# Performance work log

Measured on AMD Instinct MI355X. Metric: run time of the kernel, lower is better.

Reference implementation:

```python
import jax, jax.numpy as jnp
from jax import lax
import numpy as np
from functools import partial

B, N, T, H, L = 16, 256, 4, 128, 2
VOCAB, OUT_VOCAB, MAX_STEPS = 1000, 1000, 15


def setup_inputs() -> dict:
    key = jax.random.key(0)
    ks = jax.random.split(key, 13)
    data = jax.random.randint(ks[0], (B, N, T), 0, VOCAB)
    true_branch_nodes = jax.random.randint(ks[1], (B, N), 0, N)
    false_branch_nodes = jax.random.randint(ks[2], (B, N), 0, N)
    exit_index = jax.random.randint(ks[3], (B,), 0, N)
    steps = jax.random.randint(ks[4], (B,), 1, MAX_STEPS + 1)
    s_in = 1.0 / np.sqrt(H)
    s_cat = 1.0 / np.sqrt(2 * L * H)
    embed = jax.random.uniform(ks[5], (VOCAB, H), jnp.float32, -0.1, 0.1)
    Wi = jax.random.normal(ks[6], (L, H, 4 * H), jnp.float32) * s_in
    Wh = jax.random.normal(ks[7], (L, H, 4 * H), jnp.float32) * s_in
    b_lstm = jnp.zeros((L, 4 * H), jnp.float32)
    Wb = jax.random.normal(ks[8], (2 * L * H, 2), jnp.float32) * s_cat
    bb = jax.random.normal(ks[9], (2,), jnp.float32) * 1e-6
    Wo = jax.random.normal(ks[10], (2 * L * H, OUT_VOCAB), jnp.float32) * s_cat
    bo = jax.random.normal(ks[11], (OUT_VOCAB,), jnp.float32) * 1e-6
    return dict(data=data, true_branch_nodes=true_branch_nodes,
                false_branch_nodes=false_branch_nodes, exit_index=exit_index,
                steps=steps, embed=embed, Wi=Wi, Wh=Wh, b_lstm=b_lstm,
                Wb=Wb, bb=bb, Wo=Wo, bo=bo)


def _lstm_step(Wi_l, Wh_l, b_l, c, h, x):
    # flax LSTMCell math: gates from input (no bias) + recurrent (bias)
    z = x @ Wi_l + h @ Wh_l + b_l  # [..., 4H]
    i, f, g, o = jnp.split(z, 4, axis=-1)
    c2 = jax.nn.sigmoid(f) * c + jax.nn.sigmoid(i) * jnp.tanh(g)
    h2 = jax.nn.sigmoid(o) * jnp.tanh(c2)
    return c2, h2


def _forward(data, true_branch_nodes, false_branch_nodes, exit_index, steps,
             embed, Wi, Wh, b_lstm, Wb, bb, Wo, bo):
    emb = embed[data]                       # [B, N, T, H]
    cs = jnp.zeros((L, B, N, H), embed.dtype)
    hs = jnp.zeros((L, B, N, H), embed.dtype)
    ip = jnp.zeros((B, N), embed.dtype).at[:, 0].set(1.0)
    b_idx = jnp.arange(B)

    seg_b = jax.vmap(partial(jax.ops.segment_sum, num_segments=N))        # [B,N,...] , [B,N]
    seg_lb = jax.vmap(seg_b, in_axes=(0, None))                           # [L,B,N,H]

    def execute(cs, hs):
        # run the stacked LSTM over the T statement tokens at every node
        def tok_step(carry, x_t):
            cs, hs = carry
            inp = x_t
            nc, nh = [], []
            for l in range(L):
                c2, h2 = _lstm_step(Wi[l], Wh[l], b_lstm[l], cs[l], hs[l], inp)
                nc.append(c2); nh.append(h2)
                inp = h2
            return (jnp.stack(nc), jnp.stack(nh)), None
        (cs, hs), _ = lax.scan(tok_step, (cs, hs), jnp.moveaxis(emb, 2, 0))
        return cs, hs

    def step(carry, _):
        cs, hs, ip, idx = carry
        cs_c, hs_c = execute(cs, hs)
        # exit node keeps its previous hidden state
        cs_c = cs_c.at[:, b_idx, exit_index].set(cs[:, b_idx, exit_index])
        hs_c = hs_c.at[:, b_idx, exit_index].set(hs[:, b_idx, exit_index])
        # branch decision from concatenated (c, h) of every layer: [B, N, 2LH]
        feats = jnp.concatenate([x for l in range(L) for x in (cs_c[l], hs_c[l])], axis=-1)
        branch = jax.nn.softmax(feats @ Wb + bb, axis=-1)
        wt = branch[..., 0] * ip            # [B, N]
        wf = branch[..., 1] * ip
        ip_new = seg_b(wt, true_branch_nodes) + seg_b(wf, false_branch_nodes)
        denom = (ip_new + 1e-7)[None, :, :, None]
        def agg(h):
            return (seg_lb(h * wt[None, :, :, None], true_branch_nodes)
                    + seg_lb(h * wf[None, :, :, None], false_branch_nodes)) / denom
        cs_new, hs_new = agg(cs_c), agg(hs_c)
        live = idx < steps                   # [B]
        cs = jnp.where(live[None, :, None, None], cs_new, cs)
        hs = jnp.where(live[None, :, None, None], hs_new, hs)
        ip = jnp.where(live[:, None], ip_new, ip)
        return (cs, hs, ip, idx + 1), None

    (cs, hs, ip, _), _ = lax.scan(step, (cs, hs, ip, jnp.zeros((), jnp.int32)),
                                  None, length=MAX_STEPS)
    fc = cs[:, b_idx, exit_index]           # [L, B, H]
    fh = hs[:, b_idx, exit_index]
    final = jnp.concatenate([x for l in range(L) for x in (fc[l], fh[l])], axis=-1)
    logits = final @ Wo + bo                # [B, OUT_VOCAB]
    return logits[:, None, :]


def reference(data, true_branch_nodes, false_branch_nodes, exit_index, steps,
              embed, Wi, Wh, b_lstm, Wb, bb, Wo, bo):
    return _forward(data, true_branch_nodes, false_branch_nodes, exit_index,
                    steps, embed, Wi, Wh, b_lstm, Wb, bb, Wo, bo)
```

## Files before the change

kernel.cpp:

```cpp
#include <hip/hip_runtime.h>
#include <hip/hip_bf16.h>
#include <stdint.h>
#include <stddef.h>

static constexpr int BB = 16, NN = 256, TT = 4, HH = 128;
static constexpr int MM = BB * NN;
static constexpr int CC = 512;
static constexpr int OUTV = 1000;
static constexpr int MAXS = 15;
static constexpr int SP = 132;

typedef float f32x4 __attribute__((ext_vector_type(4)));
typedef short s16x8 __attribute__((ext_vector_type(8)));

__device__ __forceinline__ float sigf(float x) { return 1.0f / (1.0f + __expf(-x)); }
__device__ __forceinline__ float tanhr(float x) { return 2.0f / (1.0f + __expf(-2.0f * x)) - 1.0f; }
__device__ __forceinline__ unsigned short f2bu(float a) {
  return __builtin_bit_cast(unsigned short, __float2bfloat16(a));
}
__device__ __forceinline__ unsigned int packh(float a, float b) {
  return (unsigned int)f2bu(a) | ((unsigned int)f2bu(b) << 16);
}
__device__ __forceinline__ float blo(unsigned int u) { return __builtin_bit_cast(float, u << 16); }
__device__ __forceinline__ float bhi(unsigned int u) { return __builtin_bit_cast(float, u & 0xffff0000u); }


__global__ __launch_bounds__(512) void csr_kernel(const int* __restrict__ tb,
                                                  const int* __restrict__ fb,
                                                  int* __restrict__ offs,
                                                  int* __restrict__ edges) {
  const int blk = blockIdx.x;
  const int tid = threadIdx.x;
  __shared__ int cnt[256], sc[256], cur[256];
  if (tid < 256) cnt[tid] = 0;
  __syncthreads();
  const int n = tid >> 1, bit = tid & 1;
  const int tgt = bit ? fb[blk * NN + n] : tb[blk * NN + n];
  atomicAdd(&cnt[tgt], 1);
  __syncthreads();
  if (tid < 256) sc[tid] = cnt[tid];
  __syncthreads();
  for (int ofs = 1; ofs < 256; ofs <<= 1) {
    int t2 = (tid < 256 && tid >= ofs) ? sc[tid - ofs] : 0;
    __syncthreads();
    if (tid < 256) sc[tid] += t2;
    __syncthreads();
  }
  if (tid < 256) { offs[blk * NN + tid] = blk * 2 * NN + sc[tid] - cnt[tid]; cur[tid] = 0; }
  if (blk == 0 && tid == 0) offs[MM] = 2 * MM;
  __syncthreads();
  int lpos = sc[tgt] - cnt[tgt] + atomicAdd(&cur[tgt], 1);
  edges[blk * 2 * NN + lpos] = (n << 1) | bit;
}

__global__ __launch_bounds__(256) void prep_kernel(
    const float* __restrict__ Wh0, const float* __restrict__ Wi1, const float* __restrict__ Wh1,
    const float* __restrict__ embed, const float* __restrict__ Wi0, const float* __restrict__ b0,
    unsigned short* __restrict__ swz, float* __restrict__ tab) {
  const int blk = blockIdx.x;
  const int tid = threadIdx.x;
  if (blk < 768) {
    int i = blk * 256 + tid;
    int mtx = i >> 16, ii = i & 65535;
    const float* W = (mtx == 0) ? Wh0 : (mtx == 1) ? Wi1 : Wh1;
    int j = ii & 7, ln = (ii >> 3) & 63, kb = (ii >> 9) & 3, ct = ii >> 11;
    int n = ln & 15, q = ln >> 4;
    swz[i] = f2bu(W[(kb * 32 + q * 8 + j) * CC + ct * 16 + n]);
    return;
  }
  const int v0 = (blk - 768) * 8;
  __shared__ float A[8][HH];
  for (int s = tid; s < 8 * HH; s += 256) {
    int r = s >> 7, k = s & 127;
    A[r][k] = embed[(size_t)(v0 + r) * HH + k];
  }
  __syncthreads();
  const int j = tid;
  float za[8], zb[8];
  {
    float ba = b0[j], bbv = b0[j + 256];
#pragma unroll
    for (int r = 0; r < 8; ++r) { za[r] = ba; zb[r] = bbv; }
  }
#pragma unroll 4
  for (int k = 0; k < HH; ++k) {
    float wa = Wi0[k * CC + j], wb = Wi0[k * CC + j + 256];
#pragma unroll
    for (int r = 0; r < 8; ++r) { za[r] += A[r][k] * wa; zb[r] += A[r][k] * wb; }
  }
  const int T = j >> 4, nn2 = j & 15;
  const int base1 = (T & 7) * 64 + nn2 * 4 + (T >> 3);
#pragma unroll
  for (int r = 0; r < 8; ++r) {
    tab[(size_t)(v0 + r) * CC + base1] = za[r];
    tab[(size_t)(v0 + r) * CC + base1 + 2] = zb[r];
  }
}


__global__ __launch_bounds__(512) void step_kernel(
    float* __restrict__ Sc0g, float* __restrict__ Sh0g,
    float* __restrict__ Sc1g, float* __restrict__ Sh1g,
    const unsigned int* __restrict__ Pr, unsigned int* __restrict__ Pw,
    const float* __restrict__ w2R, float* __restrict__ w2W,
    const int* __restrict__ offs, const int* __restrict__ edges,
    const float* __restrict__ tab,
    const unsigned short* __restrict__ swzWh0, const unsigned short* __restrict__ swzWi1,
    const unsigned short* __restrict__ swzWh1, const float* __restrict__ b1,
    const float* __restrict__ Wb, const float* __restrict__ bb,
    const int* __restrict__ data, const int* __restrict__ exi,
    const int* __restrict__ steps, int step) {
  const int B = blockIdx.x;
  const int b = (B & 7) | (((B >> 3) & 1) << 3);
  const int g16 = B >> 4;
  const int row0 = b * NN + g16 * 16;
  const int sb = steps[b];
  const bool aggLive = (step >= 1) && ((step - 1) < sb);
  const bool lstmLive = (step < sb);
  if (!aggLive && !lstmLive) return;

  const int tid = threadIdx.x;
  const int w = tid >> 6;
  const int lane = tid & 63;
  const int n16 = lane & 15, qq = lane >> 4;
  const int kcol = w * 16 + n16;
  const int basePos = ((kcol >> 5) * 64 + ((kcol >> 3) & 3) * 16) * 8 + (kcol & 7);

  __shared__ float c0L[16 * SP], h0L[16 * SP], c1L[16 * SP], h1L[16 * SP];
  __shared__ __align__(16) unsigned short hA0[2][2048], hA1[2][2048];
  __shared__ float exitP[512];
  __shared__ float ipL[16];
  __shared__ int toks[64];

  s16x8 B0f[4][4], B1f[4][4];
  float b1v[4];
  const s16x8* pWh0 = (const s16x8*)swzWh0;
  const s16x8* pWh1 = (const s16x8*)swzWh1;
  const s16x8* pWi1 = (const s16x8*)swzWi1;
  if (lstmLive) {
#pragma unroll
    for (int g = 0; g < 4; ++g) {
      int ci = w + 8 * g;
#pragma unroll
      for (int kb = 0; kb < 4; ++kb) {
        B0f[g][kb] = pWh0[(ci * 4 + kb) * 64 + lane];
        B1f[g][kb] = pWh1[(ci * 4 + kb) * 64 + lane];
      }
      b1v[g] = b1[ci * 16 + n16];
    }
    if (tid < 64) toks[tid] = data[(row0 + (tid >> 2)) * TT + (tid & 3)];
  }

  if (aggLive) {
    const int l = tid & 31;
    const int m = tid >> 5;
    const int node = row0 + m;
    const int beg = offs[node], end = offs[node + 1];
    const float* wR = w2R + (b << 9);
    float ac0[4] = {0,0,0,0}, ah0[4] = {0,0,0,0}, ac1[4] = {0,0,0,0}, ah1[4] = {0,0,0,0};
    float wsum = 0.f;
    float wvA = 0.f, wvB = 0.f;
    uint4 pA0 = {0,0,0,0}, pA1 = {0,0,0,0}, pB0 = {0,0,0,0}, pB1 = {0,0,0,0};
    if (beg < end) {
      int rec = edges[beg];
      wvA = wR[rec];
      const uint4* pr = (const uint4*)(Pr + (size_t)((b << 8) + (rec >> 1)) * 256 + 8 * l);
      pA0 = pr[0]; pA1 = pr[1];
    }
    if (beg + 1 < end) {
      int rec = edges[beg + 1];
      wvB = wR[rec];
      const uint4* pr = (const uint4*)(Pr + (size_t)((b << 8) + (rec >> 1)) * 256 + 8 * l);
      pB0 = pr[0]; pB1 = pr[1];
    }
    for (int e = beg; e < end; e += 2) {
      float w0 = wvA; uint4 u00 = pA0, u01 = pA1;
      float w1 = wvB; uint4 u10 = pB0, u11 = pB1;
      const bool has1 = (e + 1 < end);
      if (e + 2 < end) {
        int rec = edges[e + 2];
        wvA = wR[rec];
        const uint4* pr = (const uint4*)(Pr + (size_t)((b << 8) + (rec >> 1)) * 256 + 8 * l);
        pA0 = pr[0]; pA1 = pr[1];
      }
      if (e + 3 < end) {
        int rec = edges[e + 3];
        wvB = wR[rec];
        const uint4* pr = (const uint4*)(Pr + (size_t)((b << 8) + (rec >> 1)) * 256 + 8 * l);
        pB0 = pr[0]; pB1 = pr[1];
      }
      wsum += w0;
      ac0[0] += w0 * blo(u00.x); ac0[1] += w0 * bhi(u00.x);
      ac0[2] += w0 * blo(u00.y); ac0[3] += w0 * bhi(u00.y);
      ah0[0] += w0 * blo(u00.z); ah0[1] += w0 * bhi(u00.z);
      ah0[2] += w0 * blo(u00.w); ah0[3] += w0 * bhi(u00.w);
      ac1[0] += w0 * blo(u01.x); ac1[1] += w0 * bhi(u01.x);
      ac1[2] += w0 * blo(u01.y); ac1[3] += w0 * bhi(u01.y);
      ah1[0] += w0 * blo(u01.z); ah1[1] += w0 * bhi(u01.z);
      ah1[2] += w0 * blo(u01.w); ah1[3] += w0 * bhi(u01.w);
      if (has1) {
        wsum += w1;
        ac0[0] += w1 * blo(u10.x); ac0[1] += w1 * bhi(u10.x);
        ac0[2] += w1 * blo(u10.y); ac0[3] += w1 * bhi(u10.y);
        ah0[0] += w1 * blo(u10.z); ah0[1] += w1 * bhi(u10.z);
        ah0[2] += w1 * blo(u10.w); ah0[3] += w1 * bhi(u10.w);
        ac1[0] += w1 * blo(u11.x); ac1[1] += w1 * bhi(u11.x);
        ac1[2] += w1 * blo(u11.y); ac1[3] += w1 * bhi(u11.y);
        ah1[0] += w1 * blo(u11.z); ah1[1] += w1 * bhi(u11.z);
        ah1[2] += w1 * blo(u11.w); ah1[3] += w1 * bhi(u11.w);
      }
    }
    float inv = 1.0f / (wsum + 1e-7f);
    float4 o0 = { ac0[0]*inv, ac0[1]*inv, ac0[2]*inv, ac0[3]*inv };
    float4 o1 = { ah0[0]*inv, ah0[1]*inv, ah0[2]*inv, ah0[3]*inv };
    float4 o2 = { ac1[0]*inv, ac1[1]*inv, ac1[2]*inv, ac1[3]*inv };
    float4 o3 = { ah1[0]*inv, ah1[1]*inv, ah1[2]*inv, ah1[3]*inv };
    ((float4*)c0L)[m * (SP / 4) + l] = o0;
    ((float4*)h0L)[m * (SP / 4) + l] = o1;
    ((float4*)c1L)[m * (SP / 4) + l] = o2;
    ((float4*)h1L)[m * (SP / 4) + l] = o3;
    if (l == 0) ipL[m] = wsum;
    if (!lstmLive) {
      ((float4*)Sc0g)[node * 32 + l] = o0;
      ((float4*)Sh0g)[node * 32 + l] = o1;
      ((float4*)Sc1g)[node * 32 + l] = o2;
      ((float4*)Sh1g)[node * 32 + l] = o3;
    }
  } else {
    for (int i2 = tid; i2 < 16 * HH; i2 += 512) {
      int m = i2 >> 7, k = i2 & 127;
      c0L[m * SP + k] = 0.f; h0L[m * SP + k] = 0.f;
      c1L[m * SP + k] = 0.f; h1L[m * SP + k] = 0.f;
    }
    if (tid < 16) ipL[tid] = (((row0 + tid) & (NN - 1)) == 0) ? 1.0f : 0.0f;
  }
  if (!lstmLive) return;

  const int exnode = exi[b];
  const int exm = exnode - (g16 * 16);
  __syncthreads();

  const f32x4* ptab = (const f32x4*)tab;
  f32x4 tvAll[4][4];
#pragma unroll
  for (int t = 0; t < TT; ++t)
#pragma unroll
    for (int r = 0; r < 4; ++r)
      tvAll[t][r] = ptab[(size_t)toks[(qq * 4 + r) * 4 + t] * (CC / 4) + w * 16 + n16];

  if (exm >= 0 && exm < 16 && tid < 128) {
    exitP[tid] = c0L[exm * SP + tid];
    exitP[128 + tid] = h0L[exm * SP + tid];
    exitP[256 + tid] = c1L[exm * SP + tid];
    exitP[384 + tid] = h1L[exm * SP + tid];
  }

  float c0r[4], c1r[4], h0r[4], h1r[4];
#pragma unroll
  for (int r = 0; r < 4; ++r) {
    int m = qq * 4 + r;
    c0r[r] = c0L[m * SP + kcol];
    c1r[r] = c1L[m * SP + kcol];
    h0r[r] = h0L[m * SP + kcol];
    h1r[r] = h1L[m * SP + kcol];
    hA0[0][basePos + m * 8] = f2bu(h0r[r]);
    hA1[0][basePos + m * 8] = f2bu(h1r[r]);
  }
  __syncthreads();

  int cur = 0;
#pragma unroll
  for (int t = 0; t < TT; ++t) {
    const int nxt = cur ^ 1;
    const s16x8* hA0c = (const s16x8*)hA0[cur];
    s16x8 a0[4];
#pragma unroll
    for (int kb = 0; kb < 4; ++kb) a0[kb] = hA0c[kb * 64 + lane];
    f32x4 d0[4];
#pragma unroll
    for (int g = 0; g < 4; ++g)
#pragma unroll
      for (int r = 0; r < 4; ++r)
        d0[g][r] = tvAll[t][r][g];

#pragma unroll
    for (int g = 0; g < 4; ++g)
#pragma unroll
      for (int kb = 0; kb < 4; ++kb)
        d0[g] = __builtin_amdgcn_mfma_f32_16x16x32_bf16(a0[kb], B0f[g][kb], d0[g], 0, 0, 0);

#pragma unroll
    for (int r = 0; r < 4; ++r) {
      float cn = sigf(d0[1][r]) * c0r[r] + sigf(d0[0][r]) * tanhr(d0[2][r]);
      float hn = sigf(d0[3][r]) * tanhr(cn);
      c0r[r] = cn; h0r[r] = hn;
      hA0[nxt][basePos + (qq * 4 + r) * 8] = f2bu(hn);
    }
    __syncthreads();

    const s16x8* hA0n = (const s16x8*)hA0[nxt];
    const s16x8* hA1c = (const s16x8*)hA1[cur];
    s16x8 a1a[4], a1b[4];
#pragma unroll
    for (int kb = 0; kb < 4; ++kb) {
      a1a[kb] = hA0n[kb * 64 + lane];
      a1b[kb] = hA1c[kb * 64 + lane];
    }
    f32x4 d1[4];
#pragma unroll
    for (int g = 0; g < 4; ++g) {
      int ci = w + 8 * g;
      s16x8 wi[4];
#pragma unroll
      for (int kb = 0; kb < 4; ++kb) wi[kb] = pWi1[(ci * 4 + kb) * 64 + lane];
      f32x4 d = { b1v[g], b1v[g], b1v[g], b1v[g] };
#pragma unroll
      for (int kb = 0; kb < 4; ++kb)
        d = __builtin_amdgcn_mfma_f32_16x16x32_bf16(a1a[kb], wi[kb], d, 0, 0, 0);
#pragma unroll
      for (int kb = 0; kb < 4; ++kb)
        d = __builtin_amdgcn_mfma_f32_16x16x32_bf16(a1b[kb], B1f[g][kb], d, 0, 0, 0);
      d1[g] = d;
    }

#pragma unroll
    for (int r = 0; r < 4; ++r) {
      float cn = sigf(d1[1][r]) * c1r[r] + sigf(d1[0][r]) * tanhr(d1[2][r]);
      float hn = sigf(d1[3][r]) * tanhr(cn);
      c1r[r] = cn; h1r[r] = hn;
      if (t + 1 < TT) hA1[nxt][basePos + (qq * 4 + r) * 8] = f2bu(hn);
    }
    cur = nxt;
  }

#pragma unroll
  for (int r = 0; r < 4; ++r) {
    int m = qq * 4 + r;
    c0L[m * SP + kcol] = c0r[r];
    h0L[m * SP + kcol] = h0r[r];
    c1L[m * SP + kcol] = c1r[r];
    h1L[m * SP + kcol] = h1r[r];
  }
  __syncthreads();

  {
    const int m = tid >> 5, sub = tid & 31;
    const int row = row0 + m;
    const bool isExit = (m == exm);
    float z0 = 0.f, z1 = 0.f;
#pragma unroll
    for (int u = 0; u < 16; ++u) {
      int k = u * 32 + sub;
      int seg = k >> 7, kk = k & 127;
      float fk;
      if (isExit) {
        fk = exitP[seg * 128 + kk];
      } else {
        fk = (seg == 0) ? c0L[m * SP + kk] : (seg == 1) ? h0L[m * SP + kk]
           : (seg == 2) ? c1L[m * SP + kk] : h1L[m * SP + kk];
      }
      z0 += fk * Wb[2 * k];
      z1 += fk * Wb[2 * k + 1];
    }
#pragma unroll
    for (int off = 16; off >= 1; off >>= 1) {
      z0 += __shfl_xor(z0, off);
      z1 += __shfl_xor(z1, off);
    }
    if (sub == 0) {
      z0 += bb[0]; z1 += bb[1];
      float mx = fmaxf(z0, z1);
      float e0 = __expf(z0 - mx), e1 = __expf(z1 - mx);
      float inv = 1.0f / (e0 + e1);
      float ipv = ipL[m];
      float2 wp = { e0 * inv * ipv, e1 * inv * ipv };
      ((float2*)w2W)[row] = wp;
    }
  }

  {
    const int m = tid >> 5, l = tid & 31;
    const bool ex = (m == exm);
    const int grow = row0 + m;
    float f0[4], f1[4], f2[4], f3[4];
#pragma unroll
    for (int i = 0; i < 4; ++i) {
      int k = 4 * l + i;
      f0[i] = ex ? exitP[k] : c0L[m * SP + k];
      f1[i] = ex ? exitP[128 + k] : h0L[m * SP + k];
      f2[i] = ex ? exitP[256 + k] : c1L[m * SP + k];
      f3[i] = ex ? exitP[384 + k] : h1L[m * SP + k];
    }
    uint4 o0 = { packh(f0[0], f0[1]), packh(f0[2], f0[3]),
                 packh(f1[0], f1[1]), packh(f1[2], f1[3]) };
    uint4 o1 = { packh(f2[0], f2[1]), packh(f2[2], f2[3]),
                 packh(f3[0], f3[1]), packh(f3[2], f3[3]) };
    uint4* pw = (uint4*)(Pw + (size_t)grow * 256 + 8 * l);
    pw[0] = o0; pw[1] = o1;
  }
}

__global__ void final_kernel(const float* __restrict__ Sc0, const float* __restrict__ Sh0,
                             const float* __restrict__ Sc1, const float* __restrict__ Sh1,
                             const int* __restrict__ exi, const float* __restrict__ Wo,
                             const float* __restrict__ bo, float* __restrict__ out) {
  const int b = blockIdx.x >> 2;
  const int vt = blockIdx.x & 3;
  const int tid = threadIdx.x;
  __shared__ float f[512];
  int row = b * NN + exi[b];
  if (tid < 128) {
    size_t g = (size_t)row * HH + tid;
    f[tid] = Sc0[g];
    f[128 + tid] = Sh0[g];
    f[256 + tid] = Sc1[g];
    f[384 + tid] = Sh1[g];
  }
  __syncthreads();
  if (tid < 250) {
    int v = vt * 250 + tid;
    float acc = bo[v];
#pragma unroll 8
    for (int k = 0; k < 512; ++k) acc += f[k] * Wo[(size_t)k * OUTV + v];
    out[b * OUTV + v] = acc;
  }
}

__global__ void zero_out_kernel(float* __restrict__ out, int n) {
  int i = blockIdx.x * blockDim.x + threadIdx.x;
  if (i < n) out[i] = 0.0f;
}


extern "C" void kernel_launch(void* const* d_in, const int* in_sizes, int n_in,
                              void* d_out, int out_size, void* d_ws, size_t ws_size,
                              hipStream_t stream) {
  const int* data = (const int*)d_in[0];
  const int* tb   = (const int*)d_in[1];
  const int* fb   = (const int*)d_in[2];
  const int* exi  = (const int*)d_in[3];
  const int* steps = (const int*)d_in[4];
  const float* embed = (const float*)d_in[5];
  const float* Wi = (const float*)d_in[6];
  const float* Wh = (const float*)d_in[7];
  const float* bl = (const float*)d_in[8];
  const float* Wb = (const float*)d_in[9];
  const float* bb = (const float*)d_in[10];
  const float* Wo = (const float*)d_in[11];
  const float* bo = (const float*)d_in[12];
  float* out = (float*)d_out;

  const float* Wi0 = Wi;
  const float* Wi1 = Wi + HH * CC;
  const float* Wh0 = Wh;
  const float* Wh1 = Wh + HH * CC;
  const float* b0 = bl;
  const float* b1 = bl + CC;

  float* ws = (float*)d_ws;
  size_t off = 0;
  float* tab = ws + off;  off += (size_t)1024 * CC;
  float* Sc0 = ws + off;  off += (size_t)MM * HH;
  float* Sh0 = ws + off;  off += (size_t)MM * HH;
  float* Sc1 = ws + off;  off += (size_t)MM * HH;
  float* Sh1 = ws + off;  off += (size_t)MM * HH;
  unsigned int* PA = (unsigned int*)(ws + off); off += (size_t)MM * 256;
  unsigned int* PB = (unsigned int*)(ws + off); off += (size_t)MM * 256;
  unsigned short* swz = (unsigned short*)(ws + off); off += 3 * 32768;
  float* w2A = ws + off;  off += 2 * MM;
  float* w2B = ws + off;  off += 2 * MM;
  int* offs  = (int*)(ws + off); off += MM + 16;
  int* edges = (int*)(ws + off); off += 2 * MM;
  (void)in_sizes; (void)n_in; (void)out_size;

  if (ws_size < off * sizeof(float)) {
    zero_out_kernel<<<(BB * OUTV + 255) / 256, 256, 0, stream>>>(out, BB * OUTV);
    return;
  }

  unsigned short* swzWh0 = swz;
  unsigned short* swzWi1 = swz + 65536;
  unsigned short* swzWh1 = swz + 2 * 65536;

  csr_kernel<<<BB, 512, 0, stream>>>(tb, fb, offs, edges);
  prep_kernel<<<893, 256, 0, stream>>>(Wh0, Wi1, Wh1, embed, Wi0, b0, swz, tab);

  for (int s = 0; s <= MAXS; ++s) {
    unsigned int* Pwp = (s & 1) ? PB : PA;
    const unsigned int* Prp = (s & 1) ? PA : PB;
    float* w2Wp = (s & 1) ? w2B : w2A;
    const float* w2Rp = (s & 1) ? w2A : w2B;
    step_kernel<<<MM / 16, 512, 0, stream>>>(
        Sc0, Sh0, Sc1, Sh1, Prp, Pwp,
        w2Rp, w2Wp,
        offs, edges, tab, swzWh0, swzWi1, swzWh1, b1, Wb, bb,
        data, exi, steps, s);
  }
  final_kernel<<<BB * 4, 256, 0, stream>>>(Sc0, Sh0, Sc1, Sh1, exi, Wo, bo, out);
}
```

Measured before the change: 510.0 us.

## Fuse two recurrence steps per launch with per-batch global spin barrier

Each launch now runs two consecutive graph steps instead of one, which halves the number of kernel launches. The two steps are separated by a per-batch counter barrier in global memory: the 16 blocks of each batch increment a slot, and thread 0 of each block spins on it with a timeout. State and weight buffers are read and written through relaxed agent-scope 64-bit atomics, so the data crosses between blocks through the shared cache rather than stale per-CU caches. This costs narrower loads and stores, adds spin-wait latency, and depends on all 16 blocks of a batch being resident at the same time. If the timeout ever fires, results could be wrong.

```diff
diff --git a/kernel.cpp b/kernel.cpp
--- a/kernel.cpp
+++ b/kernel.cpp
@@ -9,9 +9,11 @@
 static constexpr int OUTV = 1000;
 static constexpr int MAXS = 15;
 static constexpr int SP = 132;
+static constexpr int ND = 8;
 
 typedef float f32x4 __attribute__((ext_vector_type(4)));
 typedef short s16x8 __attribute__((ext_vector_type(8)));
+typedef unsigned long long u64;
 
 __device__ __forceinline__ float sigf(float x) { return 1.0f / (1.0f + __expf(-x)); }
 __device__ __forceinline__ float tanhr(float x) { return 2.0f / (1.0f + __expf(-2.0f * x)) - 1.0f; }
@@ -24,14 +26,26 @@
 __device__ __forceinline__ float blo(unsigned int u) { return __builtin_bit_cast(float, u << 16); }
 __device__ __forceinline__ float bhi(unsigned int u) { return __builtin_bit_cast(float, u & 0xffff0000u); }
 
+__device__ __forceinline__ u64 ld64_llc(const u64* p) {
+  return __hip_atomic_load(p, __ATOMIC_RELAXED, __HIP_MEMORY_SCOPE_AGENT);
+}
+__device__ __forceinline__ void st64_llc(u64* p, u64 v) {
+  __hip_atomic_store(p, v, __ATOMIC_RELAXED, __HIP_MEMORY_SCOPE_AGENT);
+}
+__device__ __forceinline__ float ldf_llc(const float* p) {
+  return __hip_atomic_load(p, __ATOMIC_RELAXED, __HIP_MEMORY_SCOPE_AGENT);
+}
+
 
 __global__ __launch_bounds__(512) void csr_kernel(const int* __restrict__ tb,
                                                   const int* __restrict__ fb,
                                                   int* __restrict__ offs,
-                                                  int* __restrict__ edges) {
+                                                  int* __restrict__ edges,
+                                                  unsigned int* __restrict__ bar) {
   const int blk = blockIdx.x;
   const int tid = threadIdx.x;
   __shared__ int cnt[256], sc[256], cur[256];
+  if (tid < ND) bar[tid * 16 + blk] = 0;
   if (tid < 256) cnt[tid] = 0;
   __syncthreads();
   const int n = tid >> 1, bit = tid & 1;
@@ -98,26 +112,29 @@
 }
 
 
-__global__ __launch_bounds__(512) void step_kernel(
+__global__ __launch_bounds__(512) void step2_kernel(
     float* __restrict__ Sc0g, float* __restrict__ Sh0g,
     float* __restrict__ Sc1g, float* __restrict__ Sh1g,
-    const unsigned int* __restrict__ Pr, unsigned int* __restrict__ Pw,
-    const float* __restrict__ w2R, float* __restrict__ w2W,
+    unsigned int* __restrict__ PA, unsigned int* __restrict__ PB,
+    float* __restrict__ w2A, float* __restrict__ w2B,
     const int* __restrict__ offs, const int* __restrict__ edges,
     const float* __restrict__ tab,
     const unsigned short* __restrict__ swzWh0, const unsigned short* __restrict__ swzWi1,
     const unsigned short* __restrict__ swzWh1, const float* __restrict__ b1,
     const float* __restrict__ Wb, const float* __restrict__ bb,
     const int* __restrict__ data, const int* __restrict__ exi,
-    const int* __restrict__ steps, int step) {
+    const int* __restrict__ steps, unsigned int* __restrict__ bar, int d) {
   const int B = blockIdx.x;
   const int b = (B & 7) | (((B >> 3) & 1) << 3);
   const int g16 = B >> 4;
   const int row0 = b * NN + g16 * 16;
   const int sb = steps[b];
-  const bool aggLive = (step >= 1) && ((step - 1) < sb);
-  const bool lstmLive = (step < sb);
-  if (!aggLive && !lstmLive) return;
+  const int s0 = 2 * d;
+  {
+    const bool aggA = (s0 >= 1) && ((s0 - 1) < sb);
+    const bool lstmA = (s0 < sb);
+    if (!aggA && !lstmA) return;
+  }
 
   const int tid = threadIdx.x;
   const int w = tid >> 6;
@@ -137,7 +154,7 @@
   const s16x8* pWh0 = (const s16x8*)swzWh0;
   const s16x8* pWh1 = (const s16x8*)swzWh1;
   const s16x8* pWi1 = (const s16x8*)swzWi1;
-  if (lstmLive) {
+  if (s0 < sb) {
 #pragma unroll
     for (int g = 0; g < 4; ++g) {
       int ci = w + 8 * g;
@@ -151,252 +168,300 @@
     if (tid < 64) toks[tid] = data[(row0 + (tid >> 2)) * TT + (tid & 3)];
   }
 
-  if (aggLive) {
-    const int l = tid & 31;
-    const int m = tid >> 5;
-    const int node = row0 + m;
-    const int beg = offs[node], end = offs[node + 1];
-    const float* wR = w2R + (b << 9);
-    float ac0[4] = {0,0,0,0}, ah0[4] = {0,0,0,0}, ac1[4] = {0,0,0,0}, ah1[4] = {0,0,0,0};
-    float wsum = 0.f;
-    float wvA = 0.f, wvB = 0.f;
-    uint4 pA0 = {0,0,0,0}, pA1 = {0,0,0,0}, pB0 = {0,0,0,0}, pB1 = {0,0,0,0};
-    if (beg < end) {
-      int rec = edges[beg];
-      wvA = wR[rec];
-      const uint4* pr = (const uint4*)(Pr + (size_t)((b << 8) + (rec >> 1)) * 256 + 8 * l);
-      pA0 = pr[0]; pA1 = pr[1];
-    }
-    if (beg + 1 < end) {
-      int rec = edges[beg + 1];
-      wvB = wR[rec];
-      const uint4* pr = (const uint4*)(Pr + (size_t)((b << 8) + (rec >> 1)) * 256 + 8 * l);
-      pB0 = pr[0]; pB1 = pr[1];
-    }
-    for (int e = beg; e < end; e += 2) {
-      float w0 = wvA; uint4 u00 = pA0, u01 = pA1;
-      float w1 = wvB; uint4 u10 = pB0, u11 = pB1;
-      const bool has1 = (e + 1 < end);
-      if (e + 2 < end) {
-        int rec = edges[e + 2];
-        wvA = wR[rec];
-        const uint4* pr = (const uint4*)(Pr + (size_t)((b << 8) + (rec >> 1)) * 256 + 8 * l);
-        pA0 = pr[0]; pA1 = pr[1];
-      }
-      if (e + 3 < end) {
-        int rec = edges[e + 3];
-        wvB = wR[rec];
-        const uint4* pr = (const uint4*)(Pr + (size_t)((b << 8) + (rec >> 1)) * 256 + 8 * l);
-        pB0 = pr[0]; pB1 = pr[1];
-      }
-      wsum += w0;
-      ac0[0] += w0 * blo(u00.x); ac0[1] += w0 * bhi(u00.x);
-      ac0[2] += w0 * blo(u00.y); ac0[3] += w0 * bhi(u00.y);
-      ah0[0] += w0 * blo(u00.z); ah0[1] += w0 * bhi(u00.z);
-      ah0[2] += w0 * blo(u00.w); ah0[3] += w0 * bhi(u00.w);
-      ac1[0] += w0 * blo(u01.x); ac1[1] += w0 * bhi(u01.x);
-      ac1[2] += w0 * blo(u01.y); ac1[3] += w0 * bhi(u01.y);
-      ah1[0] += w0 * blo(u01.z); ah1[1] += w0 * bhi(u01.z);
-      ah1[2] += w0 * blo(u01.w); ah1[3] += w0 * bhi(u01.w);
-      if (has1) {
-        wsum += w1;
-        ac0[0] += w1 * blo(u10.x); ac0[1] += w1 * bhi(u10.x);
-        ac0[2] += w1 * blo(u10.y); ac0[3] += w1 * bhi(u10.y);
-        ah0[0] += w1 * blo(u10.z); ah0[1] += w1 * bhi(u10.z);
-        ah0[2] += w1 * blo(u10.w); ah0[3] += w1 * bhi(u10.w);
-        ac1[0] += w1 * blo(u11.x); ac1[1] += w1 * bhi(u11.x);
-        ac1[2] += w1 * blo(u11.y); ac1[3] += w1 * bhi(u11.y);
-        ah1[0] += w1 * blo(u11.z); ah1[1] += w1 * bhi(u11.z);
-        ah1[2] += w1 * blo(u11.w); ah1[3] += w1 * bhi(u11.w);
-      }
-    }
-    float inv = 1.0f / (wsum + 1e-7f);
-    float4 o0 = { ac0[0]*inv, ac0[1]*inv, ac0[2]*inv, ac0[3]*inv };
-    float4 o1 = { ah0[0]*inv, ah0[1]*inv, ah0[2]*inv, ah0[3]*inv };
-    float4 o2 = { ac1[0]*inv, ac1[1]*inv, ac1[2]*inv, ac1[3]*inv };
-    float4 o3 = { ah1[0]*inv, ah1[1]*inv, ah1[2]*inv, ah1[3]*inv };
-    ((float4*)c0L)[m * (SP / 4) + l] = o0;
-    ((float4*)h0L)[m * (SP / 4) + l] = o1;
-    ((float4*)c1L)[m * (SP / 4) + l] = o2;
-    ((float4*)h1L)[m * (SP / 4) + l] = o3;
-    if (l == 0) ipL[m] = wsum;
-    if (!lstmLive) {
-      ((float4*)Sc0g)[node * 32 + l] = o0;
-      ((float4*)Sh0g)[node * 32 + l] = o1;
-      ((float4*)Sc1g)[node * 32 + l] = o2;
-      ((float4*)Sh1g)[node * 32 + l] = o3;
-    }
-  } else {
-    for (int i2 = tid; i2 < 16 * HH; i2 += 512) {
-      int m = i2 >> 7, k = i2 & 127;
-      c0L[m * SP + k] = 0.f; h0L[m * SP + k] = 0.f;
-      c1L[m * SP + k] = 0.f; h1L[m * SP + k] = 0.f;
-    }
-    if (tid < 16) ipL[tid] = (((row0 + tid) & (NN - 1)) == 0) ? 1.0f : 0.0f;
-  }
-  if (!lstmLive) return;
-
   const int exnode = exi[b];
   const int exm = exnode - (g16 * 16);
-  __syncthreads();
-
-  const f32x4* ptab = (const f32x4*)tab;
-  f32x4 tvAll[4][4];
-#pragma unroll
-  for (int t = 0; t < TT; ++t)
-#pragma unroll
-    for (int r = 0; r < 4; ++r)
-      tvAll[t][r] = ptab[(size_t)toks[(qq * 4 + r) * 4 + t] * (CC / 4) + w * 16 + n16];
-
-  if (exm >= 0 && exm < 16 && tid < 128) {
-    exitP[tid] = c0L[exm * SP + tid];
-    exitP[128 + tid] = h0L[exm * SP + tid];
-    exitP[256 + tid] = c1L[exm * SP + tid];
-    exitP[384 + tid] = h1L[exm * SP + tid];
-  }
-
-  float c0r[4], c1r[4], h0r[4], h1r[4];
-#pragma unroll
-  for (int r = 0; r < 4; ++r) {
-    int m = qq * 4 + r;
-    c0r[r] = c0L[m * SP + kcol];
-    c1r[r] = c1L[m * SP + kcol];
-    h0r[r] = h0L[m * SP + kcol];
-    h1r[r] = h1L[m * SP + kcol];
-    hA0[0][basePos + m * 8] = f2bu(h0r[r]);
-    hA1[0][basePos + m * 8] = f2bu(h1r[r]);
-  }
-  __syncthreads();
-
-  int cur = 0;
-#pragma unroll
-  for (int t = 0; t < TT; ++t) {
-    const int nxt = cur ^ 1;
-    const s16x8* hA0c = (const s16x8*)hA0[cur];
-    s16x8 a0[4];
-#pragma unroll
-    for (int kb = 0; kb < 4; ++kb) a0[kb] = hA0c[kb * 64 + lane];
-    f32x4 d0[4];
-#pragma unroll
-    for (int g = 0; g < 4; ++g)
+  unsigned int* barslot = bar + d * 16 + b;
+
+  for (int half = 0; half < 2; ++half) {
+    const int s = s0 + half;
+    const bool aggLive = (s >= 1) && ((s - 1) < sb);
+    const bool lstmLive = (s < sb);
+    const unsigned int* Pr = (s & 1) ? PB : PA;
+    unsigned int* Pw = (s & 1) ? PA : PB;
+    const float* w2R = (s & 1) ? w2B : w2A;
+    float* w2W = (s & 1) ? w2A : w2B;
+
+    if (half == 1) {
+      if (tid == 0) {
+        unsigned long long t0 = __builtin_amdgcn_s_memrealtime();
+        while (__hip_atomic_load(barslot, __ATOMIC_RELAXED, __HIP_MEMORY_SCOPE_AGENT) < 16u) {
+          __builtin_amdgcn_s_sleep(8);
+          if (__builtin_amdgcn_s_memrealtime() - t0 > 100000ull) break;
+        }
+      }
+      asm volatile("" ::: "memory");
+      __syncthreads();
+    }
+
+    if (aggLive) {
+      const int l = tid & 31;
+      const int m = tid >> 5;
+      const int node = row0 + m;
+      const int beg = offs[node], end = offs[node + 1];
+      const float* wR = w2R + (b << 9);
+      float ac0[4] = {0,0,0,0}, ah0[4] = {0,0,0,0}, ac1[4] = {0,0,0,0}, ah1[4] = {0,0,0,0};
+      float wsum = 0.f;
+      float wvA = 0.f, wvB = 0.f;
+      u64 a0q = 0, a1q = 0, a2q = 0, a3q = 0;
+      u64 b0q = 0, b1q = 0, b2q = 0, b3q = 0;
+      if (beg < end) {
+        int rec = edges[beg];
+        wvA = ldf_llc(&wR[rec]);
+        const u64* pr = (const u64*)(Pr + (size_t)((b << 8) + (rec >> 1)) * 256 + 8 * l);
+        a0q = ld64_llc(pr + 0); a1q = ld64_llc(pr + 1);
+        a2q = ld64_llc(pr + 2); a3q = ld64_llc(pr + 3);
+      }
+      if (beg + 1 < end) {
+        int rec = edges[beg + 1];
+        wvB = ldf_llc(&wR[rec]);
+        const u64* pr = (const u64*)(Pr + (size_t)((b << 8) + (rec >> 1)) * 256 + 8 * l);
+        b0q = ld64_llc(pr + 0); b1q = ld64_llc(pr + 1);
+        b2q = ld64_llc(pr + 2); b3q = ld64_llc(pr + 3);
+      }
+      for (int e = beg; e < end; e += 2) {
+        float w0 = wvA; u64 c0q = a0q, c1q = a1q, c2q = a2q, c3q = a3q;
+        float w1 = wvB; u64 d0q = b0q, d1q = b1q, d2q = b2q, d3q = b3q;
+        const bool has1 = (e + 1 < end);
+        if (e + 2 < end) {
+          int rec = edges[e + 2];
+          wvA = ldf_llc(&wR[rec]);
+          const u64* pr = (const u64*)(Pr + (size_t)((b << 8) + (rec >> 1)) * 256 + 8 * l);
+          a0q = ld64_llc(pr + 0); a1q = ld64_llc(pr + 1);
+          a2q = ld64_llc(pr + 2); a3q = ld64_llc(pr + 3);
+        }
+        if (e + 3 < end) {
+          int rec = edges[e + 3];
+          wvB = ldf_llc(&wR[rec]);
+          const u64* pr = (const u64*)(Pr + (size_t)((b << 8) + (rec >> 1)) * 256 + 8 * l);
+          b0q = ld64_llc(pr + 0); b1q = ld64_llc(pr + 1);
+          b2q = ld64_llc(pr + 2); b3q = ld64_llc(pr + 3);
+        }
+        {
+          unsigned int x0 = (unsigned)c0q, x1 = (unsigned)(c0q >> 32);
+          unsigned int x2 = (unsigned)c1q, x3 = (unsigned)(c1q >> 32);
+          unsigned int y0 = (unsigned)c2q, y1 = (unsigned)(c2q >> 32);
+          unsigned int y2 = (unsigned)c3q, y3 = (unsigned)(c3q >> 32);
+          wsum += w0;
+          ac0[0] += w0 * blo(x0); ac0[1] += w0 * bhi(x0);
+          ac0[2] += w0 * blo(x1); ac0[3] += w0 * bhi(x1);
+          ah0[0] += w0 * blo(x2); ah0[1] += w0 * bhi(x2);
+          ah0[2] += w0 * blo(x3); ah0[3] += w0 * bhi(x3);
+          ac1[0] += w0 * blo(y0); ac1[1] += w0 * bhi(y0);
+          ac1[2] += w0 * blo(y1); ac1[3] += w0 * bhi(y1);
+          ah1[0] += w0 * blo(y2); ah1[1] += w0 * bhi(y2);
+          ah1[2] += w0 * blo(y3); ah1[3] += w0 * bhi(y3);
+        }
+        if (has1) {
+          unsigned int x0 = (unsigned)d0q, x1 = (unsigned)(d0q >> 32);
+          unsigned int x2 = (unsigned)d1q, x3 = (unsigned)(d1q >> 32);
+          unsigned int y0 = (unsigned)d2q, y1 = (unsigned)(d2q >> 32);
+          unsigned int y2 = (unsigned)d3q, y3 = (unsigned)(d3q >> 32);
+          wsum += w1;
+          ac0[0] += w1 * blo(x0); ac0[1] += w1 * bhi(x0);
+          ac0[2] += w1 * blo(x1); ac0[3] += w1 * bhi(x1);
+          ah0[0] += w1 * blo(x2); ah0[1] += w1 * bhi(x2);
+          ah0[2] += w1 * blo(x3); ah0[3] += w1 * bhi(x3);
+          ac1[0] += w1 * blo(y0); ac1[1] += w1 * bhi(y0);
+          ac1[2] += w1 * blo(y1); ac1[3] += w1 * bhi(y1);
+          ah1[0] += w1 * blo(y2); ah1[1] += w1 * bhi(y2);
+          ah1[2] += w1 * blo(y3); ah1[3] += w1 * bhi(y3);
+        }
+      }
+      float inv = 1.0f / (wsum + 1e-7f);
+      float4 o0 = { ac0[0]*inv, ac0[1]*inv, ac0[2]*inv, ac0[3]*inv };
+      float4 o1 = { ah0[0]*inv, ah0[1]*inv, ah0[2]*inv, ah0[3]*inv };
+      float4 o2 = { ac1[0]*inv, ac1[1]*inv, ac1[2]*inv, ac1[3]*inv };
+      float4 o3 = { ah1[0]*inv, ah1[1]*inv, ah1[2]*inv, ah1[3]*inv };
+      ((float4*)c0L)[m * (SP / 4) + l] = o0;
+      ((float4*)h0L)[m * (SP / 4) + l] = o1;
+      ((float4*)c1L)[m * (SP / 4) + l] = o2;
+      ((float4*)h1L)[m * (SP / 4) + l] = o3;
+      if (l == 0) ipL[m] = wsum;
+      if (!lstmLive) {
+        ((float4*)Sc0g)[node * 32 + l] = o0;
+        ((float4*)Sh0g)[node * 32 + l] = o1;
+        ((float4*)Sc1g)[node * 32 + l] = o2;
+        ((float4*)Sh1g)[node * 32 + l] = o3;
+      }
+    } else {
+      for (int i2 = tid; i2 < 16 * HH; i2 += 512) {
+        int m = i2 >> 7, k = i2 & 127;
+        c0L[m * SP + k] = 0.f; h0L[m * SP + k] = 0.f;
+        c1L[m * SP + k] = 0.f; h1L[m * SP + k] = 0.f;
+      }
+      if (tid < 16) ipL[tid] = (((row0 + tid) & (NN - 1)) == 0) ? 1.0f : 0.0f;
+    }
+    if (!lstmLive) return;
+
+    __syncthreads();
+
+    const f32x4* ptab = (const f32x4*)tab;
+    f32x4 tvAll[4][4];
+#pragma unroll
+    for (int t = 0; t < TT; ++t)
 #pragma unroll
       for (int r = 0; r < 4; ++r)
-        d0[g][r] = tvAll[t][r][g];
-
-#pragma unroll
-    for (int g = 0; g < 4; ++g)
-#pragma unroll
-      for (int kb = 0; kb < 4; ++kb)
-        d0[g] = __builtin_amdgcn_mfma_f32_16x16x32_bf16(a0[kb], B0f[g][kb], d0[g], 0, 0, 0);
-
+        tvAll[t][r] = ptab[(size_t)toks[(qq * 4 + r) * 4 + t] * (CC / 4) + w * 16 + n16];
+
+    if (exm >= 0 && exm < 16 && tid < 128) {
+      exitP[tid] = c0L[exm * SP + tid];
+      exitP[128 + tid] = h0L[exm * SP + tid];
+      exitP[256 + tid] = c1L[exm * SP + tid];
+      exitP[384 + tid] = h1L[exm * SP + tid];
+    }
+
+    float c0r[4], c1r[4], h0r[4], h1r[4];
 #pragma unroll
     for (int r = 0; r < 4; ++r) {
-      float cn = sigf(d0[1][r]) * c0r[r] + sigf(d0[0][r]) * tanhr(d0[2][r]);
-      float hn = sigf(d0[3][r]) * tanhr(cn);
-      c0r[r] = cn; h0r[r] = hn;
-      hA0[nxt][basePos + (qq * 4 + r) * 8] = f2bu(hn);
+      int m = qq * 4 + r;
+      c0r[r] = c0L[m * SP + kcol];
+      c1r[r] = c1L[m * SP + kcol];
+      h0r[r] = h0L[m * SP + kcol];
+      h1r[r] = h1L[m * SP + kcol];
+      hA0[0][basePos + m * 8] = f2bu(h0r[r]);
+      hA1[0][basePos + m * 8] = f2bu(h1r[r]);
     }
     __syncthreads();
 
-    const s16x8* hA0n = (const s16x8*)hA0[nxt];
-    const s16x8* hA1c = (const s16x8*)hA1[cur];
-    s16x8 a1a[4], a1b[4];
-#pragma unroll
-    for (int kb = 0; kb < 4; ++kb) {
-      a1a[kb] = hA0n[kb * 64 + lane];
-      a1b[kb] = hA1c[kb * 64 + lane];
-    }
-    f32x4 d1[4];
-#pragma unroll
-    for (int g = 0; g < 4; ++g) {
-      int ci = w + 8 * g;
-      s16x8 wi[4];
-#pragma unroll
-      for (int kb = 0; kb < 4; ++kb) wi[kb] = pWi1[(ci * 4 + kb) * 64 + lane];
-      f32x4 d = { b1v[g], b1v[g], b1v[g], b1v[g] };
-#pragma unroll
-      for (int kb = 0; kb < 4; ++kb)
-        d = __builtin_amdgcn_mfma_f32_16x16x32_bf16(a1a[kb], wi[kb], d, 0, 0, 0);
-#pragma unroll
-      for (int kb = 0; kb < 4; ++kb)
-        d = __builtin_amdgcn_mfma_f32_16x16x32_bf16(a1b[kb], B1f[g][kb], d, 0, 0, 0);
-      d1[g] = d;
+    int cur = 0;
+#pragma unroll
+    for (int t = 0; t < TT; ++t) {
+      const int nxt = cur ^ 1;
+      const s16x8* hA0c = (const s16x8*)hA0[cur];
+      s16x8 a0[4];
+#pragma unroll
+      for (int kb = 0; kb < 4; ++kb) a0[kb] = hA0c[kb * 64 + lane];
+      f32x4 d0[4];
+#pragma unroll
+      for (int g = 0; g < 4; ++g)
+#pragma unroll
+        for (int r = 0; r < 4; ++r)
+          d0[g][r] = tvAll[t][r][g];
+
+#pragma unroll
+      for (int g = 0; g < 4; ++g)
+#pragma unroll
+        for (int kb = 0; kb < 4; ++kb)
+          d0[g] = __builtin_amdgcn_mfma_f32_16x16x32_bf16(a0[kb], B0f[g][kb], d0[g], 0, 0, 0);
+
+#pragma unroll
+      for (int r = 0; r < 4; ++r) {
+        float cn = sigf(d0[1][r]) * c0r[r] + sigf(d0[0][r]) * tanhr(d0[2][r]);
+        float hn = sigf(d0[3][r]) * tanhr(cn);
+        c0r[r] = cn; h0r[r] = hn;
+        hA0[nxt][basePos + (qq * 4 + r) * 8] = f2bu(hn);
+      }
+      __syncthreads();
+
+      const s16x8* hA0n = (const s16x8*)hA0[nxt];
+      const s16x8* hA1c = (const s16x8*)hA1[cur];
+      s16x8 a1a[4], a1b[4];
+#pragma unroll
+      for (int kb = 0; kb < 4; ++kb) {
+        a1a[kb] = hA0n[kb * 64 + lane];
+        a1b[kb] = hA1c[kb * 64 + lane];
+      }
+      f32x4 d1[4];
+#pragma unroll
+      for (int g = 0; g < 4; ++g) {
+        int ci = w + 8 * g;
+        s16x8 wi[4];
+#pragma unroll
+        for (int kb = 0; kb < 4; ++kb) wi[kb] = pWi1[(ci * 4 + kb) * 64 + lane];
+        f32x4 dd = { b1v[g], b1v[g], b1v[g], b1v[g] };
+#pragma unroll
+        for (int kb = 0; kb < 4; ++kb)
+          dd = __builtin_amdgcn_mfma_f32_16x16x32_bf16(a1a[kb], wi[kb], dd, 0, 0, 0);
+#pragma unroll
+        for (int kb = 0; kb < 4; ++kb)
+          dd = __builtin_amdgcn_mfma_f32_16x16x32_bf16(a1b[kb], B1f[g][kb], dd, 0, 0, 0);
+        d1[g] = dd;
+      }
+
+#pragma unroll
+      for (int r = 0; r < 4; ++r) {
+        float cn = sigf(d1[1][r]) * c1r[r] + sigf(d1[0][r]) * tanhr(d1[2][r]);
+        float hn = sigf(d1[3][r]) * tanhr(cn);
+        c1r[r] = cn; h1r[r] = hn;
+        if (t + 1 < TT) hA1[nxt][basePos + (qq * 4 + r) * 8] = f2bu(hn);
+      }
+      cur = nxt;
     }
 
 #pragma unroll
     for (int r = 0; r < 4; ++r) {
-      float cn = sigf(d1[1][r]) * c1r[r] + sigf(d1[0][r]) * tanhr(d1[2][r]);
-      float hn = sigf(d1[3][r]) * tanhr(cn);
-      c1r[r] = cn; h1r[r] = hn;
-      if (t + 1 < TT) hA1[nxt][basePos + (qq * 4 + r) * 8] = f2bu(hn);
-    }
-    cur = nxt;
-  }
-
-#pragma unroll
-  for (int r = 0; r < 4; ++r) {
-    int m = qq * 4 + r;
-    c0L[m * SP + kcol] = c0r[r];
-    h0L[m * SP + kcol] = h0r[r];
-    c1L[m * SP + kcol] = c1r[r];
-    h1L[m * SP + kcol] = h1r[r];
-  }
-  __syncthreads();
-
-  {
-    const int m = tid >> 5, sub = tid & 31;
-    const int row = row0 + m;
-    const bool isExit = (m == exm);
-    float z0 = 0.f, z1 = 0.f;
-#pragma unroll
-    for (int u = 0; u < 16; ++u) {
-      int k = u * 32 + sub;
-      int seg = k >> 7, kk = k & 127;
-      float fk;
-      if (isExit) {
-        fk = exitP[seg * 128 + kk];
-      } else {
-        fk = (seg == 0) ? c0L[m * SP + kk] : (seg == 1) ? h0L[m * SP + kk]
-           : (seg == 2) ? c1L[m * SP + kk] : h1L[m * SP + kk];
-      }
-      z0 += fk * Wb[2 * k];
-      z1 += fk * Wb[2 * k + 1];
-    }
-#pragma unroll
-    for (int off = 16; off >= 1; off >>= 1) {
-      z0 += __shfl_xor(z0, off);
-      z1 += __shfl_xor(z1, off);
-    }
-    if (sub == 0) {
-      z0 += bb[0]; z1 += bb[1];
-      float mx = fmaxf(z0, z1);
-      float e0 = __expf(z0 - mx), e1 = __expf(z1 - mx);
-      float inv = 1.0f / (e0 + e1);
-      float ipv = ipL[m];
-      float2 wp = { e0 * inv * ipv, e1 * inv * ipv };
-      ((float2*)w2W)[row] = wp;
-    }
-  }
-
-  {
-    const int m = tid >> 5, l = tid & 31;
-    const bool ex = (m == exm);
-    const int grow = row0 + m;
-    float f0[4], f1[4], f2[4], f3[4];
-#pragma unroll
-    for (int i = 0; i < 4; ++i) {
-      int k = 4 * l + i;
-      f0[i] = ex ? exitP[k] : c0L[m * SP + k];
-      f1[i] = ex ? exitP[128 + k] : h0L[m * SP + k];
-      f2[i] = ex ? exitP[256 + k] : c1L[m * SP + k];
-      f3[i] = ex ? exitP[384 + k] : h1L[m * SP + k];
-    }
-    uint4 o0 = { packh(f0[0], f0[1]), packh(f0[2], f0[3]),
-                 packh(f1[0], f1[1]), packh(f1[2], f1[3]) };
-    uint4 o1 = { packh(f2[0], f2[1]), packh(f2[2], f2[3]),
-                 packh(f3[0], f3[1]), packh(f3[2], f3[3]) };
-    uint4* pw = (uint4*)(Pw + (size_t)grow * 256 + 8 * l);
-    pw[0] = o0; pw[1] = o1;
+      int m = qq * 4 + r;
+      c0L[m * SP + kcol] = c0r[r];
+      h0L[m * SP + kcol] = h0r[r];
+      c1L[m * SP + kcol] = c1r[r];
+      h1L[m * SP + kcol] = h1r[r];
+    }
+    __syncthreads();
+
+    {
+      const int m = tid >> 5, sub = tid & 31;
+      const int row = row0 + m;
+      const bool isExit = (m == exm);
+      float z0 = 0.f, z1 = 0.f;
+#pragma unroll
+      for (int u = 0; u < 16; ++u) {
+        int k = u * 32 + sub;
+        int seg = k >> 7, kk = k & 127;
+        float fk;
+        if (isExit) {
+          fk = exitP[seg * 128 + kk];
+        } else {
+          fk = (seg == 0) ? c0L[m * SP + kk] : (seg == 1) ? h0L[m * SP + kk]
+             : (seg == 2) ? c1L[m * SP + kk] : h1L[m * SP + kk];
+        }
+        z0 += fk * Wb[2 * k];
+        z1 += fk * Wb[2 * k + 1];
+      }
+#pragma unroll
+      for (int off = 16; off >= 1; off >>= 1) {
+        z0 += __shfl_xor(z0, off);
+        z1 += __shfl_xor(z1, off);
+      }
+      if (sub == 0) {
+        z0 += bb[0]; z1 += bb[1];
+        float mx = fmaxf(z0, z1);
+        float e0 = __expf(z0 - mx), e1 = __expf(z1 - mx);
+        float inv = 1.0f / (e0 + e1);
+        float ipv = ipL[m];
+        float wt = e0 * inv * ipv, wf = e1 * inv * ipv;
+        u64 pk = ((u64)__builtin_bit_cast(unsigned int, wf) << 32)
+               | __builtin_bit_cast(unsigned int, wt);
+        st64_llc((u64*)&w2W[2 * row], pk);
+      }
+    }
+
+    {
+      const int m = tid >> 5, l = tid & 31;
+      const bool ex = (m == exm);
+      const int grow = row0 + m;
+      float f0[4], f1[4], f2[4], f3[4];
+#pragma unroll
+      for (int i = 0; i < 4; ++i) {
+        int k = 4 * l + i;
+        f0[i] = ex ? exitP[k] : c0L[m * SP + k];
+        f1[i] = ex ? exitP[128 + k] : h0L[m * SP + k];
+        f2[i] = ex ? exitP[256 + k] : c1L[m * SP + k];
+        f3[i] = ex ? exitP[384 + k] : h1L[m * SP + k];
+      }
+      u64* pw = (u64*)(Pw + (size_t)grow * 256 + 8 * l);
+      st64_llc(pw + 0, ((u64)packh(f0[2], f0[3]) << 32) | packh(f0[0], f0[1]));
+      st64_llc(pw + 1, ((u64)packh(f1[2], f1[3]) << 32) | packh(f1[0], f1[1]));
+      st64_llc(pw + 2, ((u64)packh(f2[2], f2[3]) << 32) | packh(f2[0], f2[1]));
+      st64_llc(pw + 3, ((u64)packh(f3[2], f3[3]) << 32) | packh(f3[0], f3[1]));
+    }
+
+    if (half == 0) {
+      __syncthreads();
+      if (tid == 0) {
+        asm volatile("s_waitcnt vmcnt(0)" ::: "memory");
+        __hip_atomic_fetch_add(barslot, 1u, __ATOMIC_RELAXED, __HIP_MEMORY_SCOPE_AGENT);
+      }
+    }
   }
 }
 
@@ -471,6 +536,7 @@
   float* w2B = ws + off;  off += 2 * MM;
   int* offs  = (int*)(ws + off); off += MM + 16;
   int* edges = (int*)(ws + off); off += 2 * MM;
+  unsigned int* bar = (unsigned int*)(ws + off); off += ND * 16;
   (void)in_sizes; (void)n_in; (void)out_size;
 
   if (ws_size < off * sizeof(float)) {
@@ -482,19 +548,14 @@
   unsigned short* swzWi1 = swz + 65536;
   unsigned short* swzWh1 = swz + 2 * 65536;
 
-  csr_kernel<<<BB, 512, 0, stream>>>(tb, fb, offs, edges);
+  csr_kernel<<<BB, 512, 0, stream>>>(tb, fb, offs, edges, bar);
   prep_kernel<<<893, 256, 0, stream>>>(Wh0, Wi1, Wh1, embed, Wi0, b0, swz, tab);
 
-  for (int s = 0; s <= MAXS; ++s) {
-    unsigned int* Pwp = (s & 1) ? PB : PA;
-    const unsigned int* Prp = (s & 1) ? PA : PB;
-    float* w2Wp = (s & 1) ? w2B : w2A;
-    const float* w2Rp = (s & 1) ? w2A : w2B;
-    step_kernel<<<MM / 16, 512, 0, stream>>>(
-        Sc0, Sh0, Sc1, Sh1, Prp, Pwp,
-        w2Rp, w2Wp,
+  for (int d = 0; d < ND; ++d) {
+    step2_kernel<<<MM / 16, 512, 0, stream>>>(
+        Sc0, Sh0, Sc1, Sh1, PA, PB, w2A, w2B,
         offs, edges, tab, swzWh0, swzWi1, swzWh1, b1, Wb, bb,
-        data, exi, steps, s);
+        data, exi, steps, bar, d);
   }
   final_kernel<<<BB * 4, 256, 0, stream>>>(Sc0, Sh0, Sc1, Sh1, exi, Wo, bo, out);
 }
```

New measurement: 1.085 ms. 2.13x slower.
